# Kernel optimization log

Measured on AMD Instinct MI355X. Metric: run time of the kernel, lower is better.

Reference implementation:

```python
import jax, jax.numpy as jnp
import numpy as np

N_NODES = 50000
N_EDGES = 1600000
IN_FEATS = 256
OUT_FEATS = 128
NEG_SLOPE = 0.2


def setup_inputs() -> dict:
    key = jax.random.key(0)
    k1, k2, k3, k4, k5, k6 = jax.random.split(key, 6)
    gain = np.sqrt(2.0)  # calculate_gain('relu')
    w_std = gain * np.sqrt(2.0 / (IN_FEATS + OUT_FEATS))  # xavier normal
    a_std = gain * np.sqrt(2.0 / (1 + OUT_FEATS))
    return {
        "feat": jax.random.normal(k1, (N_NODES, IN_FEATS), dtype=jnp.float32),
        "W": jax.random.normal(k2, (OUT_FEATS, IN_FEATS), dtype=jnp.float32) * w_std,
        "attn_l": jax.random.normal(k3, (1, OUT_FEATS), dtype=jnp.float32) * a_std,
        "attn_r": jax.random.normal(k4, (1, OUT_FEATS), dtype=jnp.float32) * a_std,
        "src": jax.random.randint(k5, (N_EDGES,), 0, N_NODES, dtype=jnp.int32),
        "dst": jax.random.randint(k6, (N_EDGES,), 0, N_NODES, dtype=jnp.int32),
    }


def reference(feat, W, attn_l, attn_r, src, dst):
    # h = fc(feat): [N, D]
    h = jnp.einsum("ni,di->nd", feat, W)
    # per-node attention logits
    el = jnp.sum(h * attn_l, axis=-1)  # [N]
    er = jnp.sum(h * attn_r, axis=-1)  # [N]
    # apply_edge: e_uv = el[u] + er[v], then leaky relu
    e = jax.nn.leaky_relu(el[src] + er[dst], NEG_SLOPE)  # [E]
    # edge softmax over incoming edges of each destination node
    m = jax.ops.segment_max(e, dst, num_segments=N_NODES)  # [N]
    m = jnp.where(jnp.isneginf(m), 0.0, m)  # nodes with no in-edges
    ex = jnp.exp(e - m[dst])  # [E]
    denom = jax.ops.segment_sum(ex, dst, num_segments=N_NODES)  # [N]
    alpha = ex / jnp.maximum(denom[dst], 1e-9)  # [E]
    # gspmv: rst[v] = sum_{(u->v)} alpha_uv * h[u]
    rst = jax.ops.segment_sum(h[src] * alpha[:, None], dst, num_segments=N_NODES)
    return rst
```

## Files before the change

kernel.cpp:

```cpp
#include <hip/hip_runtime.h>
#include <hip/hip_bf16.h>


#define IN_FEATS 256
#define OUT_FEATS 128
#define NBINS 256
#define CAPB_LOG 14
#define CAPB (1 << CAPB_LOG)
#define SCAT_BLOCKS 512
#define SLICE_DSTS 32
#define SCAP 2048

typedef __bf16 bf16x8 __attribute__((ext_vector_type(8)));
typedef float f32x4 __attribute__((ext_vector_type(4)));

__global__ void prep(const float* __restrict__ W, __bf16* __restrict__ Wb, int nw,
                     int* __restrict__ cur) {
    int i = blockIdx.x * 256 + threadIdx.x;
    if (i < nw) Wb[i] = (__bf16)W[i];
    if (i < NBINS) cur[i] = i << CAPB_LOG;
}

__global__ __launch_bounds__(256) void gemm_mfma(const float* __restrict__ feat,
                                                 const __bf16* __restrict__ Wb,
                                                 const float* __restrict__ attn_l,
                                                 const float* __restrict__ attn_r,
                                                 __bf16* __restrict__ hb,
                                                 float* __restrict__ el,
                                                 float* __restrict__ er, int n) {
    const int wid = threadIdx.x >> 6;
    const int lane = threadIdx.x & 63;
    const int s = lane & 15;
    const int q = lane >> 4;
    const int m0 = blockIdx.x * 64 + wid * 16;
    if (m0 >= n) return;

    const int mrow = min(m0 + s, n - 1);
    const float* arow = feat + (size_t)mrow * IN_FEATS + q * 8;

    f32x4 acc[8];
#pragma unroll
    for (int nt = 0; nt < 8; nt++) acc[nt] = (f32x4){0.f, 0.f, 0.f, 0.f};

#pragma unroll
    for (int ks = 0; ks < 8; ks++) {
        const int k0 = ks * 32;
        float4 f0 = *(const float4*)(arow + k0);
        float4 f1 = *(const float4*)(arow + k0 + 4);
        bf16x8 a;
        a[0] = (__bf16)f0.x; a[1] = (__bf16)f0.y; a[2] = (__bf16)f0.z; a[3] = (__bf16)f0.w;
        a[4] = (__bf16)f1.x; a[5] = (__bf16)f1.y; a[6] = (__bf16)f1.z; a[7] = (__bf16)f1.w;
#pragma unroll
        for (int nt = 0; nt < 8; nt++) {
            bf16x8 b = *(const bf16x8*)(Wb + (size_t)(nt * 16 + s) * IN_FEATS + k0 + q * 8);
            acc[nt] = __builtin_amdgcn_mfma_f32_16x16x32_bf16(a, b, acc[nt], 0, 0, 0);
        }
    }

    float al[8], ar[8];
#pragma unroll
    for (int nt = 0; nt < 8; nt++) {
        al[nt] = attn_l[nt * 16 + s];
        ar[nt] = attn_r[nt * 16 + s];
    }

#pragma unroll
    for (int r = 0; r < 4; r++) {
        const int row = m0 + q * 4 + r;
        const bool ok = row < n;
        float pl = 0.f, pr = 0.f;
#pragma unroll
        for (int nt = 0; nt < 8; nt++) {
            float v = acc[nt][r];
            if (ok) hb[(size_t)row * OUT_FEATS + nt * 16 + s] = (__bf16)v;
            pl += v * al[nt];
            pr += v * ar[nt];
        }
#pragma unroll
        for (int m = 1; m < 16; m <<= 1) {
            pl += __shfl_xor(pl, m);
            pr += __shfl_xor(pr, m);
        }
        if (ok && s == 0) {
            el[row] = pl;
            er[row] = pr;
        }
    }
}

__global__ __launch_bounds__(256) void scatter_kernel(const int* __restrict__ src,
                                                      const int* __restrict__ dst,
                                                      int* __restrict__ bin_cur,
                                                      unsigned* __restrict__ arena,
                                                      int E) {
    __shared__ int h[NBINS];
    __shared__ int base[NBINS];
    const int t = threadIdx.x;
    h[t] = 0;
    __syncthreads();
    const int chunk = (E + gridDim.x - 1) / gridDim.x;
    const int beg = blockIdx.x * chunk;
    const int end = min(beg + chunk, E);
    for (int i = beg + t; i < end; i += 256)
        atomicAdd(&h[dst[i] >> 8], 1);
    __syncthreads();
    if (h[t] > 0)
        base[t] = atomicAdd(&bin_cur[t], h[t]);
    h[t] = 0;
    __syncthreads();
    for (int i = beg + t; i < end; i += 256) {
        int d = dst[i];
        int bin = d >> 8;
        int pos = base[bin] + atomicAdd(&h[bin], 1);
        pos = min(pos, ((bin + 1) << CAPB_LOG) - 1);
        arena[pos] = ((unsigned)d << 16) | (unsigned)src[i];
    }
}

__global__ __launch_bounds__(256) void build_csr(const unsigned* __restrict__ arena,
                                                 const int* __restrict__ bin_cur,
                                                 const float* __restrict__ el,
                                                 const float* __restrict__ er,
                                                 unsigned* __restrict__ edges,
                                                 int* __restrict__ row_beg,
                                                 int* __restrict__ row_end,
                                                 int N, int edges_cap) {
    __shared__ int cnt[SLICE_DSTS];
    __shared__ int off[SLICE_DSTS];
    const int blk = blockIdx.x;
    const int b = blk >> 3;
    const int j = blk & 7;
    const int t = threadIdx.x;
    const int abeg = b << CAPB_LOG;
    const int aend = min(bin_cur[b], abeg + CAPB);

    if (t < SLICE_DSTS) cnt[t] = 0;
    __syncthreads();
    for (int i = abeg + t; i < aend; i += 256) {
        int d8 = (arena[i] >> 16) & 255;
        if ((d8 >> 5) == j) atomicAdd(&cnt[d8 & 31], 1);
    }
    __syncthreads();
    if (t < SLICE_DSTS) off[t] = cnt[t];
    __syncthreads();
    for (int o = 1; o < SLICE_DSTS; o <<= 1) {
        int v = (t >= o && t < SLICE_DSTS) ? off[t - o] : 0;
        __syncthreads();
        if (t < SLICE_DSTS) off[t] += v;
        __syncthreads();
    }
    int mycnt = 0, excl = 0;
    if (t < SLICE_DSTS) {
        mycnt = cnt[t];
        excl = off[t] - mycnt;
    }
    __syncthreads();
    if (t < SLICE_DSTS) off[t] = excl;
    __syncthreads();

    const int sbase = blk * SCAP;
    if (t < SLICE_DSTS) {
        int v = (b << 8) + j * SLICE_DSTS + t;
        if (v < N) {
            row_beg[v] = sbase + excl;
            row_end[v] = sbase + excl + mycnt;
        }
        cnt[t] = 0;
    }
    __syncthreads();
    for (int i = abeg + t; i < aend; i += 256) {
        unsigned e = arena[i];
        int d8 = (e >> 16) & 255;
        if ((d8 >> 5) != j) continue;
        int u = (int)(e & 0xFFFFu);
        int d = (b << 8) + d8;
        float x = el[u] + er[d];
        x = (x > 0.f) ? x : 0.2f * x;
        float w = __expf(x);
        int r = atomicAdd(&cnt[d8 & 31], 1);
        int pos = sbase + off[d8 & 31] + r;
        pos = min(pos, edges_cap - 1);
        edges[pos] = (__float_as_uint(w) & 0xFFFF0000u) | (unsigned)u;
    }
}

__global__ __launch_bounds__(256) void gat_kernel(const __bf16* __restrict__ hb,
                                                  const unsigned* __restrict__ edges,
                                                  const int* __restrict__ row_beg,
                                                  const int* __restrict__ row_end,
                                                  float* __restrict__ out, int n) {
    const int v = blockIdx.x * 4 + (threadIdx.x >> 6);
    if (v >= n) return;
    const int lane = threadIdx.x & 63;
    const int beg = row_beg[v];
    const int end = row_end[v];
    const unsigned* hbu = (const unsigned*)hb;

    float acc0 = 0.f, acc1 = 0.f, wsum = 0.f;
    for (int c0 = beg; c0 < end; c0 += 64) {
        const int nn = min(64, end - c0);
        int my = (c0 + lane < end) ? (int)edges[c0 + lane] : 0;

        int k = 0;
        for (; k + 4 <= nn; k += 4) {
#pragma unroll
            for (int tt = 0; tt < 4; tt++) {
                unsigned e = (unsigned)__shfl(my, k + tt);
                int u = (int)(e & 0xFFFFu);
                float w = __uint_as_float(e & 0xFFFF0000u);
                wsum += w;
                unsigned pair = hbu[(size_t)u * (OUT_FEATS / 2) + lane];
                acc0 += w * __uint_as_float(pair << 16);
                acc1 += w * __uint_as_float(pair & 0xffff0000u);
            }
        }
        for (; k < nn; k++) {
            unsigned e = (unsigned)__shfl(my, k);
            int u = (int)(e & 0xFFFFu);
            float w = __uint_as_float(e & 0xFFFF0000u);
            wsum += w;
            unsigned pair = hbu[(size_t)u * (OUT_FEATS / 2) + lane];
            acc0 += w * __uint_as_float(pair << 16);
            acc1 += w * __uint_as_float(pair & 0xffff0000u);
        }
    }
    const float dnm = fmaxf(wsum, 1e-9f);
    float2 o = make_float2(acc0 / dnm, acc1 / dnm);
    *(float2*)(out + (size_t)v * OUT_FEATS + lane * 2) = o;
}

extern "C" void kernel_launch(void* const* d_in, const int* in_sizes, int n_in,
                              void* d_out, int out_size, void* d_ws, size_t ws_size,
                              hipStream_t stream) {
    const float* feat   = (const float*)d_in[0];
    const float* W      = (const float*)d_in[1];
    const float* attn_l = (const float*)d_in[2];
    const float* attn_r = (const float*)d_in[3];
    const int*   src    = (const int*)d_in[4];
    const int*   dst    = (const int*)d_in[5];
    const int N = in_sizes[0] / IN_FEATS;
    const int E = in_sizes[4];
    float* out = (float*)d_out;

    char* p = (char*)d_ws;
    auto alloc = [&](size_t bytes) -> char* {
        char* r = p;
        p += (bytes + 255) & ~(size_t)255;
        return r;
    };
    const int nbuckets = (N + 255) / 256;
    const int nslices = nbuckets * 8;
    const int edges_cap = nslices * SCAP;

    __bf16* hb    = (__bf16*)alloc((size_t)N * OUT_FEATS * sizeof(__bf16));
    __bf16* Wb    = (__bf16*)alloc((size_t)OUT_FEATS * IN_FEATS * sizeof(__bf16));
    float* el     = (float*)alloc((size_t)N * sizeof(float));
    float* er     = (float*)alloc((size_t)N * sizeof(float));
    int*   bin_cur = (int*)alloc((size_t)NBINS * sizeof(int));
    int*   row_beg = (int*)alloc((size_t)N * sizeof(int));
    int*   row_end = (int*)alloc((size_t)N * sizeof(int));
    unsigned* arena = (unsigned*)alloc((size_t)NBINS * CAPB * sizeof(unsigned));
    unsigned* edges = (unsigned*)alloc((size_t)edges_cap * sizeof(unsigned));

    prep<<<dim3((OUT_FEATS * IN_FEATS + 255) / 256), dim3(256), 0, stream>>>(
        W, Wb, OUT_FEATS * IN_FEATS, bin_cur);

    gemm_mfma<<<dim3((N + 63) / 64), dim3(256), 0, stream>>>(feat, Wb, attn_l, attn_r,
                                                             hb, el, er, N);

    scatter_kernel<<<dim3(SCAT_BLOCKS), dim3(256), 0, stream>>>(src, dst, bin_cur,
                                                                arena, E);
    build_csr<<<dim3(nslices), dim3(256), 0, stream>>>(arena, bin_cur, el, er, edges,
                                                       row_beg, row_end, N, edges_cap);

    gat_kernel<<<dim3((N + 3) / 4), dim3(256), 0, stream>>>(hb, edges, row_beg,
                                                            row_end, out, N);
}
```

Baseline: 252.5 us.

## Fuse scatter into GEMM launch and build CSR per bucket in LDS

Merges the edge scatter into the GEMM kernel as extra blocks, so the two independent stages share one launch and can run concurrently. build_csr now handles one whole 256-destination bucket per 512-thread block, staging the bucket's arena entries in LDS. Previously each bucket was read 8 times, once per 32-dst slice, with a fixed-capacity output slot per slice. The gather loop in gat_kernel is unrolled by 8 instead of 4. The trade-offs are 64KB of LDS per build_csr block, which limits occupancy, and only ~196 build_csr blocks, which lowers parallelism.

After: 207.7 us. -17.7%, faster.

```diff
diff --git a/kernel.cpp b/kernel.cpp
--- a/kernel.cpp
+++ b/kernel.cpp
@@ -8,8 +8,6 @@
 #define CAPB_LOG 14
 #define CAPB (1 << CAPB_LOG)
 #define SCAT_BLOCKS 512
-#define SLICE_DSTS 32
-#define SCAP 2048
 
 typedef __bf16 bf16x8 __attribute__((ext_vector_type(8)));
 typedef float f32x4 __attribute__((ext_vector_type(4)));
@@ -21,13 +19,41 @@
     if (i < NBINS) cur[i] = i << CAPB_LOG;
 }
 
-__global__ __launch_bounds__(256) void gemm_mfma(const float* __restrict__ feat,
-                                                 const __bf16* __restrict__ Wb,
-                                                 const float* __restrict__ attn_l,
-                                                 const float* __restrict__ attn_r,
-                                                 __bf16* __restrict__ hb,
-                                                 float* __restrict__ el,
-                                                 float* __restrict__ er, int n) {
+__global__ __launch_bounds__(256) void gemm_scatter(
+    const float* __restrict__ feat, const __bf16* __restrict__ Wb,
+    const float* __restrict__ attn_l, const float* __restrict__ attn_r,
+    __bf16* __restrict__ hb, float* __restrict__ el, float* __restrict__ er,
+    const int* __restrict__ src, const int* __restrict__ dst,
+    int* __restrict__ bin_cur, unsigned* __restrict__ arena,
+    int n, int E, int G) {
+    __shared__ int h[NBINS];
+    __shared__ int base[NBINS];
+
+    if (blockIdx.x >= G) {
+        const int blk = blockIdx.x - G;
+        const int t = threadIdx.x;
+        h[t] = 0;
+        __syncthreads();
+        const int chunk = (E + SCAT_BLOCKS - 1) / SCAT_BLOCKS;
+        const int beg = blk * chunk;
+        const int end = min(beg + chunk, E);
+        for (int i = beg + t; i < end; i += 256)
+            atomicAdd(&h[dst[i] >> 8], 1);
+        __syncthreads();
+        if (h[t] > 0)
+            base[t] = atomicAdd(&bin_cur[t], h[t]);
+        h[t] = 0;
+        __syncthreads();
+        for (int i = beg + t; i < end; i += 256) {
+            int d = dst[i];
+            int bin = d >> 8;
+            int pos = base[bin] + atomicAdd(&h[bin], 1);
+            pos = min(pos, ((bin + 1) << CAPB_LOG) - 1);
+            arena[pos] = ((unsigned)d << 16) | (unsigned)src[i];
+        }
+        return;
+    }
+
     const int wid = threadIdx.x >> 6;
     const int lane = threadIdx.x & 63;
     const int s = lane & 15;
@@ -88,36 +114,7 @@
     }
 }
 
-__global__ __launch_bounds__(256) void scatter_kernel(const int* __restrict__ src,
-                                                      const int* __restrict__ dst,
-                                                      int* __restrict__ bin_cur,
-                                                      unsigned* __restrict__ arena,
-                                                      int E) {
-    __shared__ int h[NBINS];
-    __shared__ int base[NBINS];
-    const int t = threadIdx.x;
-    h[t] = 0;
-    __syncthreads();
-    const int chunk = (E + gridDim.x - 1) / gridDim.x;
-    const int beg = blockIdx.x * chunk;
-    const int end = min(beg + chunk, E);
-    for (int i = beg + t; i < end; i += 256)
-        atomicAdd(&h[dst[i] >> 8], 1);
-    __syncthreads();
-    if (h[t] > 0)
-        base[t] = atomicAdd(&bin_cur[t], h[t]);
-    h[t] = 0;
-    __syncthreads();
-    for (int i = beg + t; i < end; i += 256) {
-        int d = dst[i];
-        int bin = d >> 8;
-        int pos = base[bin] + atomicAdd(&h[bin], 1);
-        pos = min(pos, ((bin + 1) << CAPB_LOG) - 1);
-        arena[pos] = ((unsigned)d << 16) | (unsigned)src[i];
-    }
-}
-
-__global__ __launch_bounds__(256) void build_csr(const unsigned* __restrict__ arena,
+__global__ __launch_bounds__(512) void build_csr(const unsigned* __restrict__ arena,
                                                  const int* __restrict__ bin_cur,
                                                  const float* __restrict__ el,
                                                  const float* __restrict__ er,
@@ -125,60 +122,55 @@
                                                  int* __restrict__ row_beg,
                                                  int* __restrict__ row_end,
                                                  int N, int edges_cap) {
-    __shared__ int cnt[SLICE_DSTS];
-    __shared__ int off[SLICE_DSTS];
-    const int blk = blockIdx.x;
-    const int b = blk >> 3;
-    const int j = blk & 7;
+    __shared__ unsigned lds[CAPB];
+    __shared__ int cnt[256];
+    __shared__ int off[256];
+    const int b = blockIdx.x;
     const int t = threadIdx.x;
     const int abeg = b << CAPB_LOG;
-    const int aend = min(bin_cur[b], abeg + CAPB);
-
-    if (t < SLICE_DSTS) cnt[t] = 0;
-    __syncthreads();
-    for (int i = abeg + t; i < aend; i += 256) {
-        int d8 = (arena[i] >> 16) & 255;
-        if ((d8 >> 5) == j) atomicAdd(&cnt[d8 & 31], 1);
-    }
-    __syncthreads();
-    if (t < SLICE_DSTS) off[t] = cnt[t];
-    __syncthreads();
-    for (int o = 1; o < SLICE_DSTS; o <<= 1) {
-        int v = (t >= o && t < SLICE_DSTS) ? off[t - o] : 0;
-        __syncthreads();
-        if (t < SLICE_DSTS) off[t] += v;
+    const int cnt_in = min(bin_cur[b] - abeg, CAPB);
+
+    for (int i = t; i < cnt_in; i += 512) lds[i] = arena[abeg + i];
+    if (t < 256) cnt[t] = 0;
+    __syncthreads();
+
+    for (int i = t; i < cnt_in; i += 512)
+        atomicAdd(&cnt[(lds[i] >> 16) & 255], 1);
+    __syncthreads();
+    if (t < 256) off[t] = cnt[t];
+    __syncthreads();
+    for (int o = 1; o < 256; o <<= 1) {
+        int v = (t < 256 && t >= o) ? off[t - o] : 0;
+        __syncthreads();
+        if (t < 256) off[t] += v;
         __syncthreads();
     }
     int mycnt = 0, excl = 0;
-    if (t < SLICE_DSTS) {
+    if (t < 256) {
         mycnt = cnt[t];
         excl = off[t] - mycnt;
     }
     __syncthreads();
-    if (t < SLICE_DSTS) off[t] = excl;
-    __syncthreads();
-
-    const int sbase = blk * SCAP;
-    if (t < SLICE_DSTS) {
-        int v = (b << 8) + j * SLICE_DSTS + t;
+    if (t < 256) {
+        off[t] = excl;
+        int v = (b << 8) + t;
         if (v < N) {
-            row_beg[v] = sbase + excl;
-            row_end[v] = sbase + excl + mycnt;
+            row_beg[v] = abeg + excl;
+            row_end[v] = abeg + excl + mycnt;
         }
         cnt[t] = 0;
     }
     __syncthreads();
-    for (int i = abeg + t; i < aend; i += 256) {
-        unsigned e = arena[i];
+
+    for (int i = t; i < cnt_in; i += 512) {
+        unsigned e = lds[i];
         int d8 = (e >> 16) & 255;
-        if ((d8 >> 5) != j) continue;
         int u = (int)(e & 0xFFFFu);
-        int d = (b << 8) + d8;
-        float x = el[u] + er[d];
+        float x = el[u] + er[(b << 8) + d8];
         x = (x > 0.f) ? x : 0.2f * x;
         float w = __expf(x);
-        int r = atomicAdd(&cnt[d8 & 31], 1);
-        int pos = sbase + off[d8 & 31] + r;
+        int r = atomicAdd(&cnt[d8], 1);
+        int pos = abeg + off[d8] + r;
         pos = min(pos, edges_cap - 1);
         edges[pos] = (__float_as_uint(w) & 0xFFFF0000u) | (unsigned)u;
     }
@@ -202,9 +194,9 @@
         int my = (c0 + lane < end) ? (int)edges[c0 + lane] : 0;
 
         int k = 0;
-        for (; k + 4 <= nn; k += 4) {
-#pragma unroll
-            for (int tt = 0; tt < 4; tt++) {
+        for (; k + 8 <= nn; k += 8) {
+#pragma unroll
+            for (int tt = 0; tt < 8; tt++) {
                 unsigned e = (unsigned)__shfl(my, k + tt);
                 int u = (int)(e & 0xFFFFu);
                 float w = __uint_as_float(e & 0xFFFF0000u);
@@ -249,8 +241,7 @@
         return r;
     };
     const int nbuckets = (N + 255) / 256;
-    const int nslices = nbuckets * 8;
-    const int edges_cap = nslices * SCAP;
+    const int edges_cap = nbuckets * CAPB;
 
     __bf16* hb    = (__bf16*)alloc((size_t)N * OUT_FEATS * sizeof(__bf16));
     __bf16* Wb    = (__bf16*)alloc((size_t)OUT_FEATS * IN_FEATS * sizeof(__bf16));
@@ -265,13 +256,12 @@
     prep<<<dim3((OUT_FEATS * IN_FEATS + 255) / 256), dim3(256), 0, stream>>>(
         W, Wb, OUT_FEATS * IN_FEATS, bin_cur);
 
-    gemm_mfma<<<dim3((N + 63) / 64), dim3(256), 0, stream>>>(feat, Wb, attn_l, attn_r,
-                                                             hb, el, er, N);
-
-    scatter_kernel<<<dim3(SCAT_BLOCKS), dim3(256), 0, stream>>>(src, dst, bin_cur,
-                                                                arena, E);
-    build_csr<<<dim3(nslices), dim3(256), 0, stream>>>(arena, bin_cur, el, er, edges,
-                                                       row_beg, row_end, N, edges_cap);
+    const int G = (N + 63) / 64;
+    gemm_scatter<<<dim3(G + SCAT_BLOCKS), dim3(256), 0, stream>>>(
+        feat, Wb, attn_l, attn_r, hb, el, er, src, dst, bin_cur, arena, N, E, G);
+
+    build_csr<<<dim3(nbuckets), dim3(512), 0, stream>>>(arena, bin_cur, el, er, edges,
+                                                        row_beg, row_end, N, edges_cap);
 
     gat_kernel<<<dim3((N + 3) / 4), dim3(256), 0, stream>>>(hb, edges, row_beg,
                                                             row_end, out, N);
```
